# Kernel tuning notes

Hardware: AMD Instinct MI355X
Metric: run time of the kernel (lower is better)

The kernel has to match this reference:

```python
import jax, jax.numpy as jnp
import numpy as np

D = 768
H = 12
MLP = 3072
EPS = 1e-5


def _layernorm(x, g, b):
    mu = jnp.mean(x, axis=-1, keepdims=True)
    var = jnp.var(x, axis=-1, keepdims=True)
    return (x - mu) * jax.lax.rsqrt(var + EPS) * g + b


def setup_inputs() -> dict:
    key = jax.random.key(0)
    ks = jax.random.split(key, 16)
    s = 0.02
    inp = {
        "x": jax.random.normal(ks[0], (8, 1024, D), dtype=jnp.float32),
        "ln1_g": jnp.ones((D,), jnp.float32),
        "ln1_b": jnp.zeros((D,), jnp.float32),
        "Wq": jax.random.normal(ks[1], (D, D), jnp.float32) * s,
        "bq": jnp.zeros((D,), jnp.float32),
        "Wk": jax.random.normal(ks[2], (D, D), jnp.float32) * s,
        "bk": jnp.zeros((D,), jnp.float32),
        "Wv": jax.random.normal(ks[3], (D, D), jnp.float32) * s,
        "bv": jnp.zeros((D,), jnp.float32),
        "Wo": jax.random.normal(ks[4], (D, D), jnp.float32) * s,
        "bo": jnp.zeros((D,), jnp.float32),
        "ln2_g": jnp.ones((D,), jnp.float32),
        "ln2_b": jnp.zeros((D,), jnp.float32),
        "W1": jax.random.normal(ks[5], (D, MLP), jnp.float32) * s,
        "b1": jnp.zeros((MLP,), jnp.float32),
        "W2": jax.random.normal(ks[6], (MLP, D), jnp.float32) * s,
        "b2": jnp.zeros((D,), jnp.float32),
    }
    return inp


def reference(x, ln1_g, ln1_b, Wq, bq, Wk, bk, Wv, bv, Wo, bo, ln2_g, ln2_b, W1, b1, W2, b2):
    b, n, d = x.shape
    dh = d // H
    scale = 1.0 / jnp.sqrt(jnp.float32(d))  # NOTE: sqrt(input_dim), per source

    h = _layernorm(x, ln1_g, ln1_b)
    q = (h @ Wq + bq).reshape(b, n, H, dh).transpose(0, 2, 1, 3)  # bhnf
    k = (h @ Wk + bk).reshape(b, n, H, dh).transpose(0, 2, 1, 3)
    v = (h @ Wv + bv).reshape(b, n, H, dh).transpose(0, 2, 1, 3)

    score = jax.nn.softmax(jnp.einsum('bhif,bhjf->bhij', q, k) * scale, axis=-1)
    attn = jnp.einsum('bhij,bhjf->bihf', score, v).reshape(b, n, d)
    out = attn @ Wo + bo + x  # residual (dropout p=0)

    h2 = _layernorm(out, ln2_g, ln2_b)
    mlp = jax.nn.gelu(jax.nn.gelu(h2 @ W1 + b1, approximate=False) @ W2 + b2, approximate=False)
    return mlp + out
```

## Files before the change

### kernel.cpp

```cpp
#include <hip/hip_runtime.h>
#include <hip/hip_bf16.h>
#include <math.h>

typedef __bf16 bf16x8 __attribute__((ext_vector_type(8)));
typedef float f32x4 __attribute__((ext_vector_type(4)));

#define DD 768
#define HH 12
#define MLPD 3072
#define QSCALE 0.036084391824351615f

__device__ __forceinline__ float gelu_fast(float x) {
    float y = 1.5957691216057308f * x + 0.07135481283154893f * x * x * x;
    return x * __builtin_amdgcn_rcpf(1.0f + __expf(-y));
}

__device__ __forceinline__ void gload16(const void* g, void* l) {
    __builtin_amdgcn_global_load_lds(
        (const __attribute__((address_space(1))) unsigned int*)g,
        (__attribute__((address_space(3))) unsigned int*)l, 16, 0, 0);
}

__global__ __launch_bounds__(256) void wtrans_all(
    const float* __restrict__ Wq, const float* __restrict__ Wk,
    const float* __restrict__ Wv, const float* __restrict__ Wo,
    const float* __restrict__ W1, const float* __restrict__ W2,
    __bf16* __restrict__ wqkv, __bf16* __restrict__ wo,
    __bf16* __restrict__ w1, __bf16* __restrict__ w2) {
    __shared__ float tile[64][65];
    int b = blockIdx.x;
    const float* W; __bf16* Wt; int K, N, tk, tn;
    if (b < 432) {
        int wsel = b / 144, r = b - wsel * 144;
        W = wsel == 0 ? Wq : (wsel == 1 ? Wk : Wv);
        Wt = wqkv + (size_t)wsel * 768 * 768;
        K = 768; N = 768; tk = r % 12; tn = r / 12;
    } else if (b < 576) {
        int r = b - 432; W = Wo; Wt = wo; K = 768; N = 768; tk = r % 12; tn = r / 12;
    } else if (b < 1152) {
        int r = b - 576; W = W1; Wt = w1; K = 768; N = 3072; tk = r % 12; tn = r / 12;
    } else {
        int r = b - 1152; W = W2; Wt = w2; K = 3072; N = 768; tk = r % 48; tn = r / 48;
    }
    int k0 = tk * 64, n0 = tn * 64;
    int t = threadIdx.x;
    int tr = t >> 6, tc = t & 63;
#pragma unroll
    for (int i = 0; i < 16; ++i) {
        int row = i * 4 + tr;
        tile[row][tc] = W[(size_t)(k0 + row) * N + n0 + tc];
    }
    __syncthreads();
#pragma unroll
    for (int i = 0; i < 16; ++i) {
        int row = i * 4 + tr;
        Wt[(size_t)(n0 + row) * K + k0 + tc] = (__bf16)tile[tc][row];
    }
}

__global__ __launch_bounds__(64) void ln_kernel(const float* __restrict__ X,
                                                const float* __restrict__ g,
                                                const float* __restrict__ b,
                                                __bf16* __restrict__ O) {
    int row = blockIdx.x;
    int lane = threadIdx.x;
    const float* xr = X + (size_t)row * DD;
    float4 v[3];
    float s = 0.f, ss = 0.f;
#pragma unroll
    for (int i = 0; i < 3; ++i) {
        v[i] = *reinterpret_cast<const float4*>(&xr[(i * 64 + lane) * 4]);
        s += v[i].x + v[i].y + v[i].z + v[i].w;
        ss += v[i].x * v[i].x + v[i].y * v[i].y + v[i].z * v[i].z + v[i].w * v[i].w;
    }
#pragma unroll
    for (int m = 1; m < 64; m <<= 1) {
        s += __shfl_xor(s, m);
        ss += __shfl_xor(ss, m);
    }
    float mu = s * (1.0f / DD);
    float rstd = rsqrtf(ss * (1.0f / DD) - mu * mu + 1e-5f);
#pragma unroll
    for (int i = 0; i < 3; ++i) {
        int c = (i * 64 + lane) * 4;
        float4 gv = *reinterpret_cast<const float4*>(&g[c]);
        float4 bv = *reinterpret_cast<const float4*>(&b[c]);
        union { __bf16 h[4]; uint2 u; } o;
        o.h[0] = (__bf16)((v[i].x - mu) * rstd * gv.x + bv.x);
        o.h[1] = (__bf16)((v[i].y - mu) * rstd * gv.y + bv.y);
        o.h[2] = (__bf16)((v[i].z - mu) * rstd * gv.z + bv.z);
        o.h[3] = (__bf16)((v[i].w - mu) * rstd * gv.w + bv.w);
        *reinterpret_cast<uint2*>(&O[(size_t)row * DD + c]) = o.u;
    }
}

template <int EPI>
__global__ __launch_bounds__(512, 2) void gemm8(
    const __bf16* __restrict__ A, const __bf16* __restrict__ Bt,
    const float* __restrict__ b0, const float* __restrict__ b1, const float* __restrict__ b2,
    void* __restrict__ o0, void* __restrict__ o1, void* __restrict__ o2,
    int M, int N, int K) {
    extern __shared__ __bf16 lds[];
    __bf16* As = lds;
    __bf16* Bs = lds + 49152;
    const int t = threadIdx.x;
    const int w = t >> 6, lane = t & 63;
    const int wm = w >> 1, wn = w & 1;
    const int lr = lane & 15, lg = lane >> 4;
    const int m0 = blockIdx.x * 256, n0 = blockIdx.y * 128;
    const int lrow8 = lane >> 3;
    const int cSwz = ((lane & 7) ^ lrow8) * 8;

    const __bf16* aSrc = A + (size_t)(m0 + w * 32 + lrow8) * K + cSwz;
    const __bf16* bSrc = Bt + (size_t)(n0 + w * 16 + lrow8) * K + cSwz;
    const int ldsA = w * 32 * 64;
    const int ldsB = w * 16 * 64;

    const int nt = K >> 6;
    f32x4 acc[4][4] = {};

    auto stageA = [&](int T, int c) {
        gload16(aSrc + (size_t)(c * 8) * K + T * 64,
                &As[(T % 3) * 16384 + ldsA + c * 8 * 64]);
    };
    auto stageB = [&](int T, int c) {
        gload16(bSrc + (size_t)(c * 8) * K + T * 64,
                &Bs[(T % 3) * 8192 + ldsB + c * 8 * 64]);
    };

    for (int T = 0; T < 2; ++T) {
        stageA(T, 0); stageA(T, 1); stageA(T, 2); stageA(T, 3);
        stageB(T, 0); stageB(T, 1);
    }
    asm volatile("s_waitcnt vmcnt(6)" ::: "memory");
    __builtin_amdgcn_s_barrier();

    for (int T = 0; T < nt; ++T) {
        const int bufA = (T % 3) * 16384, bufB = (T % 3) * 8192;
#pragma unroll
        for (int kg = 0; kg < 2; ++kg) {
            bf16x8 af[4], bfr[4];
#pragma unroll
            for (int i = 0; i < 4; ++i)
                af[i] = *reinterpret_cast<const bf16x8*>(
                    &As[bufA + (wm * 64 + i * 16 + lr) * 64 + (((kg << 2) | lg) ^ (lr & 7)) * 8]);
#pragma unroll
            for (int j = 0; j < 4; ++j)
                bfr[j] = *reinterpret_cast<const bf16x8*>(
                    &Bs[bufB + (wn * 64 + j * 16 + lr) * 64 + (((kg << 2) | lg) ^ (lr & 7)) * 8]);
            if (T + 2 < nt) {
                stageA(T + 2, kg * 2); stageA(T + 2, kg * 2 + 1); stageB(T + 2, kg);
            }
            __builtin_amdgcn_s_barrier();
            asm volatile("s_waitcnt lgkmcnt(0)" ::: "memory");
            __builtin_amdgcn_sched_barrier(0);
            __builtin_amdgcn_s_setprio(1);
#pragma unroll
            for (int i = 0; i < 4; ++i)
#pragma unroll
                for (int j = 0; j < 4; ++j)
                    acc[i][j] = __builtin_amdgcn_mfma_f32_16x16x32_bf16(bfr[j], af[i], acc[i][j], 0, 0, 0);
            __builtin_amdgcn_s_setprio(0);
            if (kg == 1) {
                if (T < nt - 2) { asm volatile("s_waitcnt vmcnt(6)" ::: "memory"); }
                else            { asm volatile("s_waitcnt vmcnt(0)" ::: "memory"); }
            }
            __builtin_amdgcn_s_barrier();
        }
    }

#pragma unroll
    for (int i = 0; i < 4; ++i) {
        const int m = m0 + wm * 64 + i * 16 + lr;
        const int bI = m >> 10, ntok = m & 1023;
#pragma unroll
        for (int j = 0; j < 4; ++j) {
            const int n = n0 + wn * 64 + j * 16 + lg * 4;
            if (EPI == 0) {
                const int wid = n / 768;
                const int cc0 = n - wid * 768;
                const int hh = cc0 >> 6, f0 = cc0 & 63;
                const float* bsel = (wid == 0 ? b0 : (wid == 1 ? b1 : b2));
                const float4 bv = *reinterpret_cast<const float4*>(&bsel[cc0]);
                const float v0 = acc[i][j][0] + bv.x, v1 = acc[i][j][1] + bv.y;
                const float v2 = acc[i][j][2] + bv.z, v3 = acc[i][j][3] + bv.w;
                if (wid == 0) {
                    union { __bf16 h[4]; uint2 u; } pk;
                    pk.h[0] = (__bf16)(v0 * QSCALE); pk.h[1] = (__bf16)(v1 * QSCALE);
                    pk.h[2] = (__bf16)(v2 * QSCALE); pk.h[3] = (__bf16)(v3 * QSCALE);
                    *reinterpret_cast<uint2*>(
                        &((__bf16*)o0)[((((size_t)(bI * HH + hh) << 10) + ntok) << 6) + f0]) = pk.u;
                } else if (wid == 1) {
                    union { __bf16 h[4]; uint2 u; } pk;
                    pk.h[0] = (__bf16)v0; pk.h[1] = (__bf16)v1;
                    pk.h[2] = (__bf16)v2; pk.h[3] = (__bf16)v3;
                    *reinterpret_cast<uint2*>(
                        &((__bf16*)o1)[((((size_t)(bI * HH + hh) << 10) + ntok) << 6) + f0]) = pk.u;
                } else {
                    __bf16* vb = (__bf16*)o2;
                    size_t base = ((size_t)(bI * HH + hh) * 64 + f0) << 10;
                    vb[base + ntok] = (__bf16)v0;
                    vb[base + (1 << 10) + ntok] = (__bf16)v1;
                    vb[base + (2 << 10) + ntok] = (__bf16)v2;
                    vb[base + (3 << 10) + ntok] = (__bf16)v3;
                }
            } else {
                const float4 bv = *reinterpret_cast<const float4*>(&b0[n]);
                union { __bf16 h[4]; uint2 u; } pk;
                pk.h[0] = (__bf16)gelu_fast(acc[i][j][0] + bv.x);
                pk.h[1] = (__bf16)gelu_fast(acc[i][j][1] + bv.y);
                pk.h[2] = (__bf16)gelu_fast(acc[i][j][2] + bv.z);
                pk.h[3] = (__bf16)gelu_fast(acc[i][j][3] + bv.w);
                *reinterpret_cast<uint2*>(&((__bf16*)o0)[(size_t)m * MLPD + n]) = pk.u;
            }
        }
    }
}

template <int EPI>
__global__ __launch_bounds__(256, 2) void gemm_p2(
    const __bf16* __restrict__ A, const __bf16* __restrict__ Bt,
    const float* __restrict__ b0, void* __restrict__ o0,
    const float* __restrict__ resid, int M, int N, int K) {
    extern __shared__ __bf16 lds[];
    __bf16* As = lds;
    __bf16* Bs = lds + 24576;
    const int t = threadIdx.x;
    const int w = t >> 6, lane = t & 63;
    const int wm = w >> 1, wn = w & 1;
    const int lr = lane & 15, lg = lane >> 4;
    const int m0 = blockIdx.x * 128, n0 = blockIdx.y * 64;
    const int lrow8 = lane >> 3;
    const int cSwz = ((lane & 7) ^ lrow8) * 8;

    const __bf16* aSrc = A + (size_t)(m0 + w * 32 + lrow8) * K + cSwz;
    const __bf16* bSrc = Bt + (size_t)(n0 + w * 16 + lrow8) * K + cSwz;
    const int ldsA = w * 32 * 64;
    const int ldsB = w * 16 * 64;

    const int nt = K >> 6;
    f32x4 acc[4][2] = {};

    auto stageA = [&](int T, int c) {
        gload16(aSrc + (size_t)(c * 8) * K + T * 64,
                &As[(T % 3) * 8192 + ldsA + c * 8 * 64]);
    };
    auto stageB = [&](int T, int c) {
        gload16(bSrc + (size_t)(c * 8) * K + T * 64,
                &Bs[(T % 3) * 4096 + ldsB + c * 8 * 64]);
    };

    for (int T = 0; T < 2; ++T) {
        stageA(T, 0); stageA(T, 1); stageA(T, 2); stageA(T, 3);
        stageB(T, 0); stageB(T, 1);
    }
    asm volatile("s_waitcnt vmcnt(6)" ::: "memory");
    __builtin_amdgcn_s_barrier();

    for (int T = 0; T < nt; ++T) {
        const int bufA = (T % 3) * 8192, bufB = (T % 3) * 4096;
#pragma unroll
        for (int kg = 0; kg < 2; ++kg) {
            bf16x8 af[4], bfr[2];
#pragma unroll
            for (int i = 0; i < 4; ++i)
                af[i] = *reinterpret_cast<const bf16x8*>(
                    &As[bufA + (wm * 64 + i * 16 + lr) * 64 + (((kg << 2) | lg) ^ (lr & 7)) * 8]);
#pragma unroll
            for (int j = 0; j < 2; ++j)
                bfr[j] = *reinterpret_cast<const bf16x8*>(
                    &Bs[bufB + (wn * 32 + j * 16 + lr) * 64 + (((kg << 2) | lg) ^ (lr & 7)) * 8]);
            if (T + 2 < nt) {
                stageA(T + 2, kg * 2); stageA(T + 2, kg * 2 + 1); stageB(T + 2, kg);
            }
            __builtin_amdgcn_s_barrier();
            asm volatile("s_waitcnt lgkmcnt(0)" ::: "memory");
            __builtin_amdgcn_sched_barrier(0);
            __builtin_amdgcn_s_setprio(1);
#pragma unroll
            for (int i = 0; i < 4; ++i)
#pragma unroll
                for (int j = 0; j < 2; ++j)
                    acc[i][j] = __builtin_amdgcn_mfma_f32_16x16x32_bf16(bfr[j], af[i], acc[i][j], 0, 0, 0);
            __builtin_amdgcn_s_setprio(0);
            if (kg == 1) {
                if (T < nt - 2) { asm volatile("s_waitcnt vmcnt(6)" ::: "memory"); }
                else            { asm volatile("s_waitcnt vmcnt(0)" ::: "memory"); }
            }
            __builtin_amdgcn_s_barrier();
        }
    }

#pragma unroll
    for (int i = 0; i < 4; ++i) {
        const int m = m0 + wm * 64 + i * 16 + lr;
#pragma unroll
        for (int j = 0; j < 2; ++j) {
            const int n = n0 + wn * 32 + j * 16 + lg * 4;
            const float4 bv = *reinterpret_cast<const float4*>(&b0[n]);
            const float v0 = acc[i][j][0] + bv.x, v1 = acc[i][j][1] + bv.y;
            const float v2 = acc[i][j][2] + bv.z, v3 = acc[i][j][3] + bv.w;
            const float4 rv = *reinterpret_cast<const float4*>(&resid[(size_t)m * DD + n]);
            if (EPI == 2) {
                float4 ov = {v0 + rv.x, v1 + rv.y, v2 + rv.z, v3 + rv.w};
                *reinterpret_cast<float4*>(&((float*)o0)[(size_t)m * DD + n]) = ov;
            } else {
                float4 ov = {gelu_fast(v0) + rv.x, gelu_fast(v1) + rv.y,
                             gelu_fast(v2) + rv.z, gelu_fast(v3) + rv.w};
                *reinterpret_cast<float4*>(&((float*)o0)[(size_t)m * DD + n]) = ov;
            }
        }
    }
}

__global__ __launch_bounds__(512, 6) void attn_kernel(
    const __bf16* __restrict__ Q, const __bf16* __restrict__ Kg,
    const __bf16* __restrict__ Vt, __bf16* __restrict__ Aout) {
    __shared__ char KsB[2][64 * 128];
    __shared__ char VsB[2][64 * 128];
    __shared__ char PsB[8][16 * 128];
    const int id = blockIdx.x;
    const int swz = (id & 7) * 96 + (id >> 3);
    const int bh = swz >> 3, qt = swz & 7;
    const int t = threadIdx.x, w = t >> 6, lane = t & 63;
    const int lr = lane & 15, lg = lane >> 4;
    const size_t bhN = (size_t)bh << 10;
    const int q0 = qt * 128;

    bf16x8 qf[2];
#pragma unroll
    for (int kg = 0; kg < 2; ++kg)
        qf[kg] = *reinterpret_cast<const bf16x8*>(&Q[(bhN + q0 + w * 16 + lr) * 64 + kg * 32 + lg * 8]);

    const int srow = t >> 3;
    const int sc = ((t & 7) ^ (srow & 7)) * 16;
    const char* kbase = (const char*)Kg + bhN * 128;
    const char* vbase = (const char*)Vt + ((size_t)bh << 17);
    const int wlds = w * 1024;

    f32x4 oacc[4] = {};
    float lsum[4] = {0.f, 0.f, 0.f, 0.f};

    gload16(kbase + (size_t)srow * 128 + sc, KsB[0] + wlds);
    gload16(vbase + (size_t)srow * 2048 + sc, VsB[0] + wlds);

    for (int kt = 0; kt < 16; ++kt) {
        const int buf = kt & 1;
        if (kt < 15) {
            gload16(kbase + (size_t)((kt + 1) * 64 + srow) * 128 + sc, KsB[buf ^ 1] + wlds);
            gload16(vbase + (size_t)srow * 2048 + (kt + 1) * 128 + sc, VsB[buf ^ 1] + wlds);
            asm volatile("s_waitcnt vmcnt(2)" ::: "memory");
        } else {
            asm volatile("s_waitcnt vmcnt(0)" ::: "memory");
        }
        __builtin_amdgcn_s_barrier();

        f32x4 s[4] = {};
        __builtin_amdgcn_s_setprio(1);
#pragma unroll
        for (int kg = 0; kg < 2; ++kg) {
#pragma unroll
            for (int j = 0; j < 4; ++j) {
                int row = j * 16 + lr;
                bf16x8 kf = *reinterpret_cast<const bf16x8*>(
                    KsB[buf] + ((row * 128 + kg * 64 + lg * 16) ^ ((row & 7) << 4)));
                s[j] = __builtin_amdgcn_mfma_f32_16x16x32_bf16(qf[kg], kf, s[j], 0, 0, 0);
            }
        }
        __builtin_amdgcn_s_setprio(0);
#pragma unroll
        for (int r = 0; r < 4; ++r) {
            int prow = lg * 4 + r;
#pragma unroll
            for (int j = 0; j < 4; ++j) {
                float pv = __expf(s[j][r]);
                lsum[r] += pv;
                *reinterpret_cast<__bf16*>(
                    PsB[w] + ((prow * 128 + (j * 16 + lr) * 2) ^ ((prow & 7) << 4))) = (__bf16)pv;
            }
        }
        __builtin_amdgcn_s_setprio(1);
#pragma unroll
        for (int kg = 0; kg < 2; ++kg) {
            bf16x8 pf = *reinterpret_cast<const bf16x8*>(
                PsB[w] + ((lr * 128 + kg * 64 + lg * 16) ^ ((lr & 7) << 4)));
#pragma unroll
            for (int j = 0; j < 4; ++j) {
                int row = j * 16 + lr;
                bf16x8 vf = *reinterpret_cast<const bf16x8*>(
                    VsB[buf] + ((row * 128 + kg * 64 + lg * 16) ^ ((row & 7) << 4)));
                oacc[j] = __builtin_amdgcn_mfma_f32_16x16x32_bf16(pf, vf, oacc[j], 0, 0, 0);
            }
        }
        __builtin_amdgcn_s_setprio(0);
        __builtin_amdgcn_s_barrier();
    }

#pragma unroll
    for (int r = 0; r < 4; ++r)
#pragma unroll
        for (int m = 1; m < 16; m <<= 1) lsum[r] += __shfl_xor(lsum[r], m);

    const int bI = bh / HH, hh = bh % HH;
#pragma unroll
    for (int r = 0; r < 4; ++r) {
        float inv = 1.0f / lsum[r];
        int qrow = q0 + w * 16 + lg * 4 + r;
        size_t base = ((size_t)(bI << 10) + qrow) * DD + hh * 64;
#pragma unroll
        for (int j = 0; j < 4; ++j)
            Aout[base + j * 16 + lr] = (__bf16)(oacc[j][r] * inv);
    }
}

extern "C" void kernel_launch(void* const* d_in, const int* in_sizes, int n_in,
                              void* d_out, int out_size, void* d_ws, size_t ws_size,
                              hipStream_t stream) {
    const float* x     = (const float*)d_in[0];
    const float* ln1_g = (const float*)d_in[1];
    const float* ln1_b = (const float*)d_in[2];
    const float* Wq    = (const float*)d_in[3];
    const float* bq    = (const float*)d_in[4];
    const float* Wk    = (const float*)d_in[5];
    const float* bk    = (const float*)d_in[6];
    const float* Wv    = (const float*)d_in[7];
    const float* bv    = (const float*)d_in[8];
    const float* Wo    = (const float*)d_in[9];
    const float* bo    = (const float*)d_in[10];
    const float* ln2_g = (const float*)d_in[11];
    const float* ln2_b = (const float*)d_in[12];
    const float* W1    = (const float*)d_in[13];
    const float* b1    = (const float*)d_in[14];
    const float* W2    = (const float*)d_in[15];
    const float* b2    = (const float*)d_in[16];

    char* p = (char*)d_ws;
    auto alloc = [&](size_t bytes) { char* r = p; p += bytes; return r; };
    __bf16* wqkv_t = (__bf16*)alloc((size_t)2304 * 768 * 2);
    __bf16* wo_t   = (__bf16*)alloc((size_t)768 * 768 * 2);
    __bf16* w1_t   = (__bf16*)alloc((size_t)3072 * 768 * 2);
    __bf16* w2_t   = (__bf16*)alloc((size_t)768 * 3072 * 2);
    __bf16* h      = (__bf16*)alloc((size_t)8192 * 768 * 2);
    float*  outb   = (float*) alloc((size_t)8192 * 768 * 4);
    __bf16* q      = (__bf16*)alloc((size_t)8192 * 768 * 2);
    __bf16* kb     = (__bf16*)alloc((size_t)8192 * 768 * 2);
    __bf16* vt     = (__bf16*)alloc((size_t)8192 * 768 * 2);
    __bf16* attn   = (__bf16*)alloc((size_t)8192 * 768 * 2);
    __bf16* mid    = q;

    const int LDS8 = 147456;
    const int LDSP = 73728;
    hipFuncSetAttribute(reinterpret_cast<const void*>(gemm8<0>),
                        hipFuncAttributeMaxDynamicSharedMemorySize, LDS8);
    hipFuncSetAttribute(reinterpret_cast<const void*>(gemm8<3>),
                        hipFuncAttributeMaxDynamicSharedMemorySize, LDS8);
    hipFuncSetAttribute(reinterpret_cast<const void*>(gemm_p2<2>),
                        hipFuncAttributeMaxDynamicSharedMemorySize, LDSP);
    hipFuncSetAttribute(reinterpret_cast<const void*>(gemm_p2<4>),
                        hipFuncAttributeMaxDynamicSharedMemorySize, LDSP);

    wtrans_all<<<1728, 256, 0, stream>>>(Wq, Wk, Wv, Wo, W1, W2, wqkv_t, wo_t, w1_t, w2_t);

    ln_kernel<<<8192, 64, 0, stream>>>(x, ln1_g, ln1_b, h);
    gemm8<0><<<dim3(32, 18), 512, LDS8, stream>>>(h, wqkv_t, bq, bk, bv, q, kb, vt,
                                                  8192, 2304, 768);
    attn_kernel<<<768, 512, 0, stream>>>(q, kb, vt, attn);
    gemm_p2<2><<<dim3(64, 12), 256, LDSP, stream>>>(attn, wo_t, bo, outb, x, 8192, 768, 768);
    ln_kernel<<<8192, 64, 0, stream>>>(outb, ln2_g, ln2_b, h);
    gemm8<3><<<dim3(32, 24), 512, LDS8, stream>>>(h, w1_t, b1, nullptr, nullptr, mid,
                                                  nullptr, nullptr, 8192, 3072, 768);
    gemm_p2<4><<<dim3(64, 12), 256, LDSP, stream>>>(mid, w2_t, b2, (float*)d_out, outb,
                                                    8192, 768, 3072);
}
```

Baseline: 257.6 us.

## Widen N-tile of output-projection GEMMs to 128 with double-buffered pipeline

The Wo and W2 GEMMs now use 128x128 output tiles per block instead of 128x64, which doubles the MFMA work per wave and raises operand reuse. The 3-stage pipeline with per-half-step staging is replaced by a simpler 2-stage double buffer that issues the whole next tile before computing the current one, with one wait and barrier per K step. This halves the grid to 384 blocks, which may underfill the CU count on this device, and the shallower prefetch exposes more load latency.

```diff
diff --git a/kernel.cpp b/kernel.cpp
--- a/kernel.cpp
+++ b/kernel.cpp
@@ -218,85 +218,78 @@
 }
 
 template <int EPI>
-__global__ __launch_bounds__(256, 2) void gemm_p2(
+__global__ __launch_bounds__(256, 2) void gemm_p3(
     const __bf16* __restrict__ A, const __bf16* __restrict__ Bt,
     const float* __restrict__ b0, void* __restrict__ o0,
     const float* __restrict__ resid, int M, int N, int K) {
     extern __shared__ __bf16 lds[];
     __bf16* As = lds;
-    __bf16* Bs = lds + 24576;
+    __bf16* Bs = lds + 16384;
     const int t = threadIdx.x;
     const int w = t >> 6, lane = t & 63;
     const int wm = w >> 1, wn = w & 1;
     const int lr = lane & 15, lg = lane >> 4;
-    const int m0 = blockIdx.x * 128, n0 = blockIdx.y * 64;
+    const int m0 = blockIdx.x * 128, n0 = blockIdx.y * 128;
     const int lrow8 = lane >> 3;
     const int cSwz = ((lane & 7) ^ lrow8) * 8;
 
     const __bf16* aSrc = A + (size_t)(m0 + w * 32 + lrow8) * K + cSwz;
-    const __bf16* bSrc = Bt + (size_t)(n0 + w * 16 + lrow8) * K + cSwz;
-    const int ldsA = w * 32 * 64;
-    const int ldsB = w * 16 * 64;
+    const __bf16* bSrc = Bt + (size_t)(n0 + w * 32 + lrow8) * K + cSwz;
+    const int ldsW = w * 32 * 64;
 
     const int nt = K >> 6;
-    f32x4 acc[4][2] = {};
-
-    auto stageA = [&](int T, int c) {
-        gload16(aSrc + (size_t)(c * 8) * K + T * 64,
-                &As[(T % 3) * 8192 + ldsA + c * 8 * 64]);
+    f32x4 acc[4][4] = {};
+
+    auto stage = [&](int T) {
+        const int buf = (T & 1) * 8192;
+#pragma unroll
+        for (int c = 0; c < 4; ++c)
+            gload16(aSrc + (size_t)(c * 8) * K + T * 64, &As[buf + ldsW + c * 8 * 64]);
+#pragma unroll
+        for (int c = 0; c < 4; ++c)
+            gload16(bSrc + (size_t)(c * 8) * K + T * 64, &Bs[buf + ldsW + c * 8 * 64]);
     };
-    auto stageB = [&](int T, int c) {
-        gload16(bSrc + (size_t)(c * 8) * K + T * 64,
-                &Bs[(T % 3) * 4096 + ldsB + c * 8 * 64]);
-    };
-
-    for (int T = 0; T < 2; ++T) {
-        stageA(T, 0); stageA(T, 1); stageA(T, 2); stageA(T, 3);
-        stageB(T, 0); stageB(T, 1);
-    }
-    asm volatile("s_waitcnt vmcnt(6)" ::: "memory");
-    __builtin_amdgcn_s_barrier();
-
+
+    stage(0);
     for (int T = 0; T < nt; ++T) {
-        const int bufA = (T % 3) * 8192, bufB = (T % 3) * 4096;
+        if (T + 1 < nt) {
+            stage(T + 1);
+            asm volatile("s_waitcnt vmcnt(8)" ::: "memory");
+        } else {
+            asm volatile("s_waitcnt vmcnt(0)" ::: "memory");
+        }
+        __builtin_amdgcn_s_barrier();
+        const int buf = (T & 1) * 8192;
 #pragma unroll
         for (int kg = 0; kg < 2; ++kg) {
-            bf16x8 af[4], bfr[2];
+            bf16x8 af[4], bfr[4];
 #pragma unroll
             for (int i = 0; i < 4; ++i)
                 af[i] = *reinterpret_cast<const bf16x8*>(
-                    &As[bufA + (wm * 64 + i * 16 + lr) * 64 + (((kg << 2) | lg) ^ (lr & 7)) * 8]);
-#pragma unroll
-            for (int j = 0; j < 2; ++j)
+                    &As[buf + (wm * 64 + i * 16 + lr) * 64 + (((kg << 2) | lg) ^ (lr & 7)) * 8]);
+#pragma unroll
+            for (int j = 0; j < 4; ++j)
                 bfr[j] = *reinterpret_cast<const bf16x8*>(
-                    &Bs[bufB + (wn * 32 + j * 16 + lr) * 64 + (((kg << 2) | lg) ^ (lr & 7)) * 8]);
-            if (T + 2 < nt) {
-                stageA(T + 2, kg * 2); stageA(T + 2, kg * 2 + 1); stageB(T + 2, kg);
-            }
-            __builtin_amdgcn_s_barrier();
+                    &Bs[buf + (wn * 64 + j * 16 + lr) * 64 + (((kg << 2) | lg) ^ (lr & 7)) * 8]);
             asm volatile("s_waitcnt lgkmcnt(0)" ::: "memory");
             __builtin_amdgcn_sched_barrier(0);
             __builtin_amdgcn_s_setprio(1);
 #pragma unroll
             for (int i = 0; i < 4; ++i)
 #pragma unroll
-                for (int j = 0; j < 2; ++j)
+                for (int j = 0; j < 4; ++j)
                     acc[i][j] = __builtin_amdgcn_mfma_f32_16x16x32_bf16(bfr[j], af[i], acc[i][j], 0, 0, 0);
             __builtin_amdgcn_s_setprio(0);
-            if (kg == 1) {
-                if (T < nt - 2) { asm volatile("s_waitcnt vmcnt(6)" ::: "memory"); }
-                else            { asm volatile("s_waitcnt vmcnt(0)" ::: "memory"); }
-            }
-            __builtin_amdgcn_s_barrier();
-        }
+        }
+        __builtin_amdgcn_s_barrier();
     }
 
 #pragma unroll
     for (int i = 0; i < 4; ++i) {
         const int m = m0 + wm * 64 + i * 16 + lr;
 #pragma unroll
-        for (int j = 0; j < 2; ++j) {
-            const int n = n0 + wn * 32 + j * 16 + lg * 4;
+        for (int j = 0; j < 4; ++j) {
+            const int n = n0 + wn * 64 + j * 16 + lg * 4;
             const float4 bv = *reinterpret_cast<const float4*>(&b0[n]);
             const float v0 = acc[i][j][0] + bv.x, v1 = acc[i][j][1] + bv.y;
             const float v2 = acc[i][j][2] + bv.z, v3 = acc[i][j][3] + bv.w;
@@ -449,14 +442,14 @@
     __bf16* mid    = q;
 
     const int LDS8 = 147456;
-    const int LDSP = 73728;
+    const int LDSP = 65536;
     hipFuncSetAttribute(reinterpret_cast<const void*>(gemm8<0>),
                         hipFuncAttributeMaxDynamicSharedMemorySize, LDS8);
     hipFuncSetAttribute(reinterpret_cast<const void*>(gemm8<3>),
                         hipFuncAttributeMaxDynamicSharedMemorySize, LDS8);
-    hipFuncSetAttribute(reinterpret_cast<const void*>(gemm_p2<2>),
+    hipFuncSetAttribute(reinterpret_cast<const void*>(gemm_p3<2>),
                         hipFuncAttributeMaxDynamicSharedMemorySize, LDSP);
-    hipFuncSetAttribute(reinterpret_cast<const void*>(gemm_p2<4>),
+    hipFuncSetAttribute(reinterpret_cast<const void*>(gemm_p3<4>),
                         hipFuncAttributeMaxDynamicSharedMemorySize, LDSP);
 
     wtrans_all<<<1728, 256, 0, stream>>>(Wq, Wk, Wv, Wo, W1, W2, wqkv_t, wo_t, w1_t, w2_t);
@@ -465,10 +458,10 @@
     gemm8<0><<<dim3(32, 18), 512, LDS8, stream>>>(h, wqkv_t, bq, bk, bv, q, kb, vt,
                                                   8192, 2304, 768);
     attn_kernel<<<768, 512, 0, stream>>>(q, kb, vt, attn);
-    gemm_p2<2><<<dim3(64, 12), 256, LDSP, stream>>>(attn, wo_t, bo, outb, x, 8192, 768, 768);
+    gemm_p3<2><<<dim3(64, 6), 256, LDSP, stream>>>(attn, wo_t, bo, outb, x, 8192, 768, 768);
     ln_kernel<<<8192, 64, 0, stream>>>(outb, ln2_g, ln2_b, h);
     gemm8<3><<<dim3(32, 24), 512, LDS8, stream>>>(h, w1_t, b1, nullptr, nullptr, mid,
                                                   nullptr, nullptr, 8192, 3072, 768);
-    gemm_p2<4><<<dim3(64, 12), 256, LDSP, stream>>>(mid, w2_t, b2, (float*)d_out, outb,
-                                                    8192, 768, 3072);
-}
+    gemm_p3<4><<<dim3(64, 6), 256, LDSP, stream>>>(mid, w2_t, b2, (float*)d_out, outb,
+                                                   8192, 768, 3072);
+}
```

New measurement: 247.2 us. 1.04x faster.
